# Kernel tuning notes

Measured on AMD Instinct MI355X. Metric: run time of the kernel, lower is better.

The kernel has to match this reference:

```python
import jax, jax.numpy as jnp
import numpy as np

B, D_IN = 16384, 1024
NUM_LAYERS, K, CB_DIM = 4, 1024, 512


def setup_inputs() -> dict:
    key = jax.random.key(0)
    ks = jax.random.split(key, 6)
    return {
        "dense_content_embedding": jax.random.normal(ks[0], (B, D_IN), jnp.float32),
        "enc_W": jax.random.normal(ks[1], (D_IN, CB_DIM), jnp.float32) / np.sqrt(D_IN),
        "enc_b": jnp.zeros((CB_DIM,), jnp.float32),
        "codebooks": jax.random.normal(ks[2], (NUM_LAYERS, K, CB_DIM), jnp.float32),
        "dec_W": jax.random.normal(ks[3], (NUM_LAYERS, CB_DIM), jnp.float32) / np.sqrt(NUM_LAYERS),
        "dec_b": jnp.zeros((CB_DIM,), jnp.float32),
    }


def reference(dense_content_embedding, enc_W, enc_b, codebooks, dec_W, dec_b):
    # encoder: Dense(codebook_dim)
    r0 = dense_content_embedding @ enc_W + enc_b  # [B, CB_DIM]

    def step(residual, cb):
        # squared L2 distance: ||r||^2 - 2 r.c + ||c||^2  -> [B, K]
        d = (jnp.sum(residual * residual, axis=-1, keepdims=True)
             - 2.0 * (residual @ cb.T)
             + jnp.sum(cb * cb, axis=-1))
        idx = jnp.argmin(d, axis=-1)            # [B]
        next_residual = residual - cb[idx]      # gather + residual update
        return next_residual, idx

    _, ids = jax.lax.scan(step, r0, codebooks)  # ids: [L, B]
    semantic_ids = ids.T                        # [B, L] (stack along axis=1)

    # decoder: Dense(codebook_dim) applied to the integer ids (as in source)
    recon = semantic_ids.astype(r0.dtype) @ dec_W + dec_b  # [B, CB_DIM]
    return recon, semantic_ids
```

## Files before the change

### kernel.cpp

```cpp
#include <hip/hip_runtime.h>
#include <float.h>
#include <limits.h>

#define BB 16384
#define DIN 1024
#define CB 512
#define KC 1024
#define NL 4

#define DELTA 0.25f

typedef __attribute__((ext_vector_type(8))) _Float16 half8;
typedef __attribute__((ext_vector_type(8))) short bf16x8;
typedef __attribute__((ext_vector_type(4))) float f32x4;

__device__ __forceinline__ unsigned short f2h(float f) {
  _Float16 h = (_Float16)f;
  return *(unsigned short*)&h;
}

__device__ __forceinline__ unsigned short f2b(float f) {
  unsigned u = __float_as_uint(f);
  unsigned r = u + 0x7fffu + ((u >> 16) & 1u);
  return (unsigned short)(r >> 16);
}
__device__ __forceinline__ float b2f(unsigned short h) {
  return __uint_as_float(((unsigned)h) << 16);
}

__device__ __forceinline__ unsigned cvtpk_bf16(float a, float b) {
  unsigned r;
  asm("v_cvt_pk_bf16_f32 %0, %1, %2" : "=v"(r) : "v"(a), "v"(b));
  return r;
}

__device__ __forceinline__ size_t staged_off(int row, int k) {
  return ((size_t)(row >> 4) * 16 + (k >> 5)) * 512 +
         (((k >> 3) & 3) * 16 + (row & 15)) * 8 + (k & 7);
}

__device__ __forceinline__ size_t staged_off_w(int row, int k) {
  return ((size_t)(row >> 4) * 32 + (k >> 5)) * 512 +
         (((k >> 3) & 3) * 16 + (row & 15)) * 8 + (k & 7);
}


__global__ __launch_bounds__(256) void cbsplit_kernel(
    const float* __restrict__ cbs, unsigned short* __restrict__ Ch16) {
  int g = (blockIdx.x * 256 + threadIdx.x) * 4;
  int k = g & (CB - 1);
  int lr = g >> 9;
  int layer = lr >> 10, row = lr & (KC - 1);
  float4 v = *(const float4*)(cbs + g);
  size_t off = (size_t)layer * (KC / 16) * 8192 + staged_off(row, k);
  *(ushort4*)(Ch16 + off) = make_ushort4(f2h(v.x), f2h(v.y), f2h(v.z), f2h(v.w));
}

__global__ __launch_bounds__(256) void wsplit_kernel(
    const float* __restrict__ W, unsigned short* __restrict__ WTh,
    unsigned short* __restrict__ WTm) {
  int g = blockIdx.x * 256 + threadIdx.x;
  int n = g >> 8;
  int k0 = (g & 255) * 4;
  ushort4 h4, m4;
  unsigned short* hp = (unsigned short*)&h4;
  unsigned short* mp = (unsigned short*)&m4;
#pragma unroll
  for (int i = 0; i < 4; ++i) {
    float x = W[(size_t)(k0 + i) * CB + n];
    unsigned short h = f2b(x);
    hp[i] = h;
    mp[i] = f2b(x - b2f(h));
  }
  size_t off = staged_off_w(n, k0);
  *(ushort4*)(WTh + off) = h4;
  *(ushort4*)(WTm + off) = m4;
}

__global__ __launch_bounds__(256) void cnorm_kernel(
    const float* __restrict__ cbs, double* __restrict__ cnorm,
    float* __restrict__ cnormF) {
  int gw = (blockIdx.x * blockDim.x + threadIdx.x) >> 6;
  int lane = threadIdx.x & 63;
  if (gw >= NL * KC) return;
  const float* row = cbs + (size_t)gw * CB;
  double s = 0.0;
  for (int i = lane; i < CB; i += 64) {
    double v = (double)row[i];
    s += v * v;
  }
#pragma unroll
  for (int off = 32; off > 0; off >>= 1)
    s += __shfl_down(s, off, 64);
  if (lane == 0) { cnorm[gw] = s; cnormF[gw] = (float)s; }
}

__global__ __launch_bounds__(256, 2) void enc_gemm(
    const float* __restrict__ X, const unsigned short* __restrict__ WTh,
    const unsigned short* __restrict__ WTm, const float* __restrict__ bias,
    float* __restrict__ R, unsigned short* __restrict__ Rh16) {
  __shared__ __align__(16) char lds[32768];
  int tid = threadIdx.x;
  int wave = tid >> 6, lane = tid & 63;
  int wm = wave >> 1, wn = wave & 1;
  int q = lane >> 4, l15 = lane & 15;
  int bx = blockIdx.x;
  int rb = ((bx & 7) << 1) + ((bx >> 3) & 1) + ((bx >> 6) << 4);
  int cbk = (bx >> 4) & 3;
  int row0 = rb * 128, n0 = cbk * 128;

  int ar = tid >> 1;
  int aq = (tid & 1) * 16;
  const float* xsrc = X + (size_t)(row0 + ar) * DIN + aq;
  int awoff = (ar >> 4) * 1024 + (((aq >> 3) & 3) * 16 + (ar & 15)) * 16;

  const char* bph = (const char*)WTh +
                    ((size_t)((n0 >> 4) + wn * 4) * 32) * 1024 + lane * 16;
  const char* bpm = (const char*)WTm +
                    ((size_t)((n0 >> 4) + wn * 4) * 32) * 1024 + lane * 16;

  f32x4 acc[4][4];
#pragma unroll
  for (int i = 0; i < 4; ++i)
#pragma unroll
    for (int j = 0; j < 4; ++j)
      acc[i][j] = (f32x4){0.f, 0.f, 0.f, 0.f};

  float xv[16];
  unsigned hp[8], mp[8];
  uint4 BHa[4], BMa[4], BHb[4], BMb[4];

#define LOADX(c)                                         \
  {                                                      \
    _Pragma("unroll") for (int j = 0; j < 4; ++j) {      \
      float4 v = *(const float4*)(xsrc + (c) * 32 + j * 4); \
      xv[4 * j + 0] = v.x; xv[4 * j + 1] = v.y;          \
      xv[4 * j + 2] = v.z; xv[4 * j + 3] = v.w;          \
    }                                                    \
  }
#define SPLITX()                                            \
  {                                                         \
    _Pragma("unroll") for (int j = 0; j < 8; ++j) {         \
      float x0 = xv[2 * j], x1 = xv[2 * j + 1];             \
      unsigned h = cvtpk_bf16(x0, x1);                      \
      float h0 = __uint_as_float(h << 16);                  \
      float h1 = __uint_as_float(h & 0xffff0000u);          \
      hp[j] = h;                                            \
      mp[j] = cvtpk_bf16(x0 - h0, x1 - h1);                 \
    }                                                       \
  }
#define WRITEA(bufbase)                                                     \
  {                                                                         \
    *(uint4*)(lds + (bufbase) + awoff) =                                    \
        make_uint4(hp[0], hp[1], hp[2], hp[3]);                             \
    *(uint4*)(lds + (bufbase) + awoff + 256) =                              \
        make_uint4(hp[4], hp[5], hp[6], hp[7]);                             \
    *(uint4*)(lds + (bufbase) + awoff + 8192) =                             \
        make_uint4(mp[0], mp[1], mp[2], mp[3]);                             \
    *(uint4*)(lds + (bufbase) + awoff + 8192 + 256) =                       \
        make_uint4(mp[4], mp[5], mp[6], mp[7]);                             \
  }
#define BLOADTO(ktile, BH, BM)                                              \
  {                                                                         \
    _Pragma("unroll") for (int tj = 0; tj < 4; ++tj) {                      \
      BH[tj] = *(const uint4*)(bph + (size_t)tj * 32768 + (size_t)(ktile) * 1024); \
      BM[tj] = *(const uint4*)(bpm + (size_t)tj * 32768 + (size_t)(ktile) * 1024); \
    }                                                                       \
  }
#define ESTEP(kt, CB_, NB_, BHc, BMc, BHn, BMn)                             \
  {                                                                         \
    if ((kt) < 31) {                                                        \
      WRITEA(NB_);                                                          \
      BLOADTO((kt) + 1, BHn, BMn);                                          \
    }                                                                       \
    if ((kt) < 30) LOADX((kt) + 2);                                         \
    const char* cb0 = lds + (CB_);                                          \
    bf16x8 ah[4], am[4];                                                    \
    _Pragma("unroll") for (int ti = 0; ti < 4; ++ti) {                      \
      ah[ti] = *(const bf16x8*)(cb0 + (wm * 4 + ti) * 1024 + lane * 16);    \
      am[ti] = *(const bf16x8*)(cb0 + 8192 + (wm * 4 + ti) * 1024 + lane * 16); \
    }                                                                       \
    _Pragma("unroll") for (int tj = 0; tj < 4; ++tj) {                      \
      bf16x8 bh = *(const bf16x8*)&BHc[tj];                                 \
      bf16x8 bm = *(const bf16x8*)&BMc[tj];                                 \
      _Pragma("unroll") for (int ti = 0; ti < 4; ++ti)                      \
        acc[ti][tj] = __builtin_amdgcn_mfma_f32_16x16x32_bf16(ah[ti], bh, acc[ti][tj], 0, 0, 0); \
      _Pragma("unroll") for (int ti = 0; ti < 4; ++ti)                      \
        acc[ti][tj] = __builtin_amdgcn_mfma_f32_16x16x32_bf16(am[ti], bh, acc[ti][tj], 0, 0, 0); \
      _Pragma("unroll") for (int ti = 0; ti < 4; ++ti)                      \
        acc[ti][tj] = __builtin_amdgcn_mfma_f32_16x16x32_bf16(ah[ti], bm, acc[ti][tj], 0, 0, 0); \
    }                                                                       \
    if ((kt) < 30) SPLITX();                                                \
    __syncthreads();                                                        \
  }

  LOADX(0); SPLITX();
  WRITEA(0);
  BLOADTO(0, BHa, BMa);
  LOADX(1); SPLITX();
  __syncthreads();

  for (int kt2 = 0; kt2 < 16; ++kt2) {
    ESTEP(2 * kt2,     0,     16384, BHa, BMa, BHb, BMb);
    ESTEP(2 * kt2 + 1, 16384, 0,     BHb, BMb, BHa, BMa);
  }

#pragma unroll
  for (int ti = 0; ti < 4; ++ti) {
#pragma unroll
    for (int tj = 0; tj < 4; ++tj) {
      int col = n0 + wn * 64 + tj * 16 + l15;
      float bv = bias[col];
#pragma unroll
      for (int r = 0; r < 4; ++r) {
        int row = row0 + wm * 64 + ti * 16 + q * 4 + r;
        float val = acc[ti][tj][r] + bv;
        R[(size_t)row * CB + col] = val;
        Rh16[staged_off(row, col)] = f2h(val);
      }
    }
  }
#undef LOADX
#undef SPLITX
#undef WRITEA
#undef BLOADTO
#undef ESTEP
}

__global__ __launch_bounds__(256, 2) void vq_stage1(
    const unsigned short* __restrict__ Rh16,
    const unsigned short* __restrict__ Ch16,
    const float* __restrict__ cnormF, float4* __restrict__ cand) {
  __shared__ __align__(16) char lds[49152];
  int tid = threadIdx.x;
  int wave = tid >> 6, lane = tid & 63;
  int q = lane >> 4, l15 = lane & 15;
  int g = blockIdx.x;
  int rb = (g & 7) + ((g >> 6) << 3);
  int cbk = (g >> 3) & 7;
  int row0 = rb * 256, n0 = cbk * 128;

  f32x4 acc[4][8];
#pragma unroll
  for (int i = 0; i < 4; ++i)
#pragma unroll
    for (int j = 0; j < 8; ++j)
      acc[i][j] = (f32x4){0.f, 0.f, 0.f, 0.f};

  const unsigned short* gA =
      Rh16 + ((size_t)(row0 >> 4) + wave * 4) * 8192 + lane * 8;
  const unsigned short* gB =
      Ch16 + ((size_t)(n0 >> 4) + wave * 2) * 8192 + lane * 8;
  char* lA = lds + wave * 4 * 1024;
  char* lB = lds + 16384 + wave * 2 * 1024;

#define STAGE1_ISSUE(ktile, bufbase)                                         \
  {                                                                          \
    _Pragma("unroll") for (int s = 0; s < 4; ++s) {                          \
      __builtin_amdgcn_global_load_lds(                                      \
          (const __attribute__((address_space(1))) void*)(                   \
              gA + (size_t)s * 8192 + (ktile) * 512),                        \
          (__attribute__((address_space(3))) void*)(lA + (bufbase) + s * 1024), \
          16, 0, 0);                                                         \
    }                                                                        \
    _Pragma("unroll") for (int s = 0; s < 2; ++s) {                          \
      __builtin_amdgcn_global_load_lds(                                      \
          (const __attribute__((address_space(1))) void*)(                   \
              gB + (size_t)s * 8192 + (ktile) * 512),                        \
          (__attribute__((address_space(3))) void*)(lB + (bufbase) + s * 1024), \
          16, 0, 0);                                                         \
    }                                                                        \
  }

  STAGE1_ISSUE(0, 0);
  __syncthreads();

  for (int kt = 0; kt < 16; ++kt) {
    int cur = kt & 1;
    if (kt < 15) STAGE1_ISSUE(kt + 1, (cur ^ 1) * 24576);
    const char* ca = lds + cur * 24576;
    const char* cbp = ca + 16384;
    half8 af[4];
#pragma unroll
    for (int ri = 0; ri < 4; ++ri)
      af[ri] = *(const half8*)(ca + (wave * 4 + ri) * 1024 + lane * 16);
#pragma unroll
    for (int tj = 0; tj < 8; ++tj) {
      half8 b = *(const half8*)(cbp + tj * 1024 + lane * 16);
#pragma unroll
      for (int ri = 0; ri < 4; ++ri)
        acc[ri][tj] = __builtin_amdgcn_mfma_f32_16x16x32_f16(af[ri], b, acc[ri][tj], 0, 0, 0);
    }
    __syncthreads();
  }
#undef STAGE1_ISSUE

  float cn[8]; int coln[8];
#pragma unroll
  for (int tj = 0; tj < 8; ++tj) {
    coln[tj] = n0 + tj * 16 + l15;
    cn[tj] = cnormF[coln[tj]];
  }
#pragma unroll
  for (int ri = 0; ri < 4; ++ri) {
#pragma unroll
    for (int r = 0; r < 4; ++r) {
      unsigned long long k1 = ~0ull, k2 = ~0ull;
#pragma unroll
      for (int tj = 0; tj < 8; ++tj) {
        float v = cn[tj] - 2.0f * acc[ri][tj][r];
        unsigned u = __float_as_uint(v);
        u = (u & 0x80000000u) ? ~u : (u | 0x80000000u);
        unsigned long long key =
            ((unsigned long long)u << 32) | (unsigned)coln[tj];
        if (key < k1) { k2 = k1; k1 = key; }
        else if (key < k2) { k2 = key; }
      }
#pragma unroll
      for (int mask = 1; mask <= 8; mask <<= 1) {
        unsigned long long o1 = __shfl_xor(k1, mask, 64);
        unsigned long long o2 = __shfl_xor(k2, mask, 64);
        if (o1 < k1) { k2 = (k1 < o2) ? k1 : o2; k1 = o1; }
        else { k2 = (k2 < o1) ? k2 : o1; }
      }
      if (l15 == 0) {
        unsigned s1 = (unsigned)(k1 >> 32), s2 = (unsigned)(k2 >> 32);
        unsigned b1 = (s1 & 0x80000000u) ? (s1 ^ 0x80000000u) : ~s1;
        unsigned b2 = (s2 & 0x80000000u) ? (s2 ^ 0x80000000u) : ~s2;
        int row = row0 + wave * 64 + ri * 16 + q * 4 + r;
        cand[(size_t)row * 8 + cbk] = make_float4(
            __uint_as_float(b1), __int_as_float((int)(unsigned)k1),
            __uint_as_float(b2), __int_as_float((int)(unsigned)k2));
      }
    }
  }
}

__global__ __launch_bounds__(256) void vq_refine(
    const float* __restrict__ cb, const double* __restrict__ cnorm,
    const float4* __restrict__ cand, float* __restrict__ R,
    unsigned short* __restrict__ Rh16, float* __restrict__ idsF, int layer,
    const float* __restrict__ decW, const float* __restrict__ decb,
    float* __restrict__ recon) {
  __shared__ int sIdx[32][16];
  __shared__ int sCnt[32];
  __shared__ int sBest[32];
  __shared__ int sPair[512];
  __shared__ int sNP;
  __shared__ double sD[32][16];

  int tid = threadIdx.x;
  int b = blockIdx.x;
  int v = ((b & 7) << 3) + ((b >> 3) & 7) + ((b >> 6) << 6);
  int row0 = v * 32;

  if (tid == 0) sNP = 0;
  __syncthreads();

  if (tid < 32) {
    int row = row0 + tid;
    float vv[16]; int ix[16];
#pragma unroll
    for (int c = 0; c < 8; ++c) {
      float4 e = cand[(size_t)row * 8 + c];
      vv[2 * c] = e.x;     ix[2 * c] = __float_as_int(e.y);
      vv[2 * c + 1] = e.z; ix[2 * c + 1] = __float_as_int(e.w);
    }
    float M = FLT_MAX; int I = INT_MAX;
#pragma unroll
    for (int p = 0; p < 16; ++p)
      if (vv[p] < M || (vv[p] == M && ix[p] < I)) { M = vv[p]; I = ix[p]; }
    int cnt = 0;
#pragma unroll
    for (int p = 0; p < 16; ++p)
      if (vv[p] < M + DELTA && cnt < 16) sIdx[tid][cnt++] = ix[p];
    sCnt[tid] = cnt;
    sBest[tid] = I;
    if (cnt >= 2) {
      int base = atomicAdd(&sNP, cnt);
      for (int c = 0; c < cnt; ++c) sPair[base + c] = (tid << 4) | c;
    }
  }
  __syncthreads();

  int np = sNP;
  int wave = tid >> 6, lane = tid & 63;
  for (int p = wave; p < np; p += 4) {
    int pr = sPair[p];
    int r = pr >> 4, c = pr & 15;
    int idx = sIdx[r][c];
    const float* rrow = R + (size_t)(row0 + r) * CB;
    const float* crow = cb + (size_t)idx * CB;
    double s = 0.0;
#pragma unroll
    for (int e = 0; e < CB; e += 64)
      s += (double)rrow[e + lane] * (double)crow[e + lane];
#pragma unroll
    for (int off = 32; off > 0; off >>= 1)
      s += __shfl_xor(s, off, 64);
    if (lane == 0) sD[r][c] = cnorm[idx] - 2.0 * s;
  }
  __syncthreads();

  if (tid < 32) {
    int cnt = sCnt[tid];
    if (cnt >= 2) {
      double bestD = 1e300; int bestI = INT_MAX;
      for (int c = 0; c < cnt; ++c) {
        double d = sD[tid][c]; int idx = sIdx[tid][c];
        if (d < bestD || (d == bestD && idx < bestI)) { bestD = d; bestI = idx; }
      }
      sBest[tid] = bestI;
    }
    idsF[(size_t)(row0 + tid) * NL + layer] = (float)sBest[tid];
  }
  __syncthreads();

  if (layer != NL - 1) {
    for (int it = tid; it < 32 * (CB / 4); it += 256) {
      int r = it >> 7, dq = (it & 127) * 4;
      int row = row0 + r;
      size_t o = (size_t)row * CB + dq;
      float4 rv = *(const float4*)(R + o);
      const float* crow = cb + (size_t)sBest[r] * CB + dq;
      float nv[4] = {rv.x - crow[0], rv.y - crow[1], rv.z - crow[2], rv.w - crow[3]};
      *(float4*)(R + o) = make_float4(nv[0], nv[1], nv[2], nv[3]);
      size_t so = staged_off(row, dq);
      *(ushort4*)(Rh16 + so) =
          make_ushort4(f2h(nv[0]), f2h(nv[1]), f2h(nv[2]), f2h(nv[3]));
    }
  } else {
    for (int it = tid; it < 32 * (CB / 4); it += 256) {
      int r = it >> 7, j0 = (it & 127) * 4;
      int row = row0 + r;
      float id3 = (float)sBest[r];
      float out[4];
#pragma unroll
      for (int e = 0; e < 4; ++e) {
        int j = j0 + e;
        float s = decb[j];
#pragma unroll
        for (int l = 0; l < NL - 1; ++l)
          s += idsF[(size_t)row * NL + l] * decW[l * CB + j];
        s += id3 * decW[(NL - 1) * CB + j];
        out[e] = s;
      }
      *(float4*)(recon + (size_t)row * CB + j0) =
          make_float4(out[0], out[1], out[2], out[3]);
    }
  }
}

extern "C" void kernel_launch(void* const* d_in, const int* in_sizes, int n_in,
                              void* d_out, int out_size, void* d_ws, size_t ws_size,
                              hipStream_t stream) {
  const float* X    = (const float*)d_in[0];
  const float* encW = (const float*)d_in[1];
  const float* encb = (const float*)d_in[2];
  const float* cbs  = (const float*)d_in[3];
  const float* decW = (const float*)d_in[4];
  const float* decb = (const float*)d_in[5];

  float* out = (float*)d_out;
  float* recon = out;
  float* idsF = out + (size_t)BB * CB;

  char* ws = (char*)d_ws;
  float* R = (float*)ws;                     ws += (size_t)BB * CB * 4;
  unsigned short* Rh16 = (unsigned short*)ws; ws += (size_t)BB * CB * 2;
  unsigned short* Ch16 = (unsigned short*)ws; ws += (size_t)NL * KC * CB * 2;
  double* cnorm = (double*)ws;               ws += (size_t)NL * KC * 8;
  float* cnormF = (float*)ws;                ws += (size_t)NL * KC * 4;
  float4* cand = (float4*)ws;                ws += (size_t)BB * 8 * 16;
  unsigned short* WTh = (unsigned short*)ws; ws += (size_t)CB * DIN * 2;
  unsigned short* WTm = (unsigned short*)ws;

  cbsplit_kernel<<<(NL * KC * CB) / 1024, 256, 0, stream>>>(cbs, Ch16);
  cnorm_kernel<<<(NL * KC) / 4, 256, 0, stream>>>(cbs, cnorm, cnormF);
  wsplit_kernel<<<(CB * DIN / 4) / 256, 256, 0, stream>>>(encW, WTh, WTm);
  enc_gemm<<<(BB / 128) * (CB / 128), 256, 0, stream>>>(X, WTh, WTm, encb, R, Rh16);
  for (int l = 0; l < NL; ++l) {
    const float* cbl = cbs + (size_t)l * KC * CB;
    vq_stage1<<<(BB / 256) * 8, 256, 0, stream>>>(
        Rh16, Ch16 + (size_t)l * KC * CB, cnormF + (size_t)l * KC, cand);
    vq_refine<<<BB / 32, 256, 0, stream>>>(cbl, cnorm + (size_t)l * KC, cand,
                                           R, Rh16, idsF, l, decW, decb, recon);
  }
}
```

Before: 358.6 us.

## Load stage-1 MFMA operands directly from global into registers, dropping LDS staging

The vq_stage1 distance GEMM no longer stages A and B tiles through double-buffered shared memory with global_load_lds and block barriers. Each wave now loads its own fragments straight from global memory into registers, using register double buffering across k-tiles. This removes the LDS traffic and per-iteration __syncthreads. The cost is that every wave loads the full 128-column B tile itself, which raises global/L2 traffic roughly fourfold for B, and it adds register pressure (24 extra uint4 per thread) under launch_bounds(256,2).

```diff
diff --git a/kernel.cpp b/kernel.cpp
--- a/kernel.cpp
+++ b/kernel.cpp
@@ -231,7 +231,6 @@
     const unsigned short* __restrict__ Rh16,
     const unsigned short* __restrict__ Ch16,
     const float* __restrict__ cnormF, float4* __restrict__ cand) {
-  __shared__ __align__(16) char lds[49152];
   int tid = threadIdx.x;
   int wave = tid >> 6, lane = tid & 63;
   int q = lane >> 4, l15 = lane & 15;
@@ -247,53 +246,48 @@
     for (int j = 0; j < 8; ++j)
       acc[i][j] = (f32x4){0.f, 0.f, 0.f, 0.f};
 
-  const unsigned short* gA =
-      Rh16 + ((size_t)(row0 >> 4) + wave * 4) * 8192 + lane * 8;
-  const unsigned short* gB =
-      Ch16 + ((size_t)(n0 >> 4) + wave * 2) * 8192 + lane * 8;
-  char* lA = lds + wave * 4 * 1024;
-  char* lB = lds + 16384 + wave * 2 * 1024;
-
-#define STAGE1_ISSUE(ktile, bufbase)                                         \
+  const char* aptr = (const char*)Rh16 +
+                     ((size_t)(row0 >> 4) + wave * 4) * 16384 + lane * 16;
+  const char* bptr = (const char*)Ch16 +
+                     ((size_t)(n0 >> 4)) * 16384 + lane * 16;
+
+  uint4 Aa[4], Ab[4];
+  uint4 Ba[8], Bb[8];
+
+#define ALOADTO(ktile, A)                                                    \
   {                                                                          \
-    _Pragma("unroll") for (int s = 0; s < 4; ++s) {                          \
-      __builtin_amdgcn_global_load_lds(                                      \
-          (const __attribute__((address_space(1))) void*)(                   \
-              gA + (size_t)s * 8192 + (ktile) * 512),                        \
-          (__attribute__((address_space(3))) void*)(lA + (bufbase) + s * 1024), \
-          16, 0, 0);                                                         \
+    _Pragma("unroll") for (int ri = 0; ri < 4; ++ri)                         \
+      A[ri] = *(const uint4*)(aptr + (size_t)ri * 16384 + (size_t)(ktile) * 1024); \
+  }
+#define BLOADTO(ktile, B)                                                    \
+  {                                                                          \
+    _Pragma("unroll") for (int tj = 0; tj < 8; ++tj)                         \
+      B[tj] = *(const uint4*)(bptr + (size_t)tj * 16384 + (size_t)(ktile) * 1024); \
+  }
+#define S1STEP(kt, Ac, Bc, An, Bn)                                           \
+  {                                                                          \
+    if ((kt) < 15) {                                                         \
+      ALOADTO((kt) + 1, An);                                                 \
+      BLOADTO((kt) + 1, Bn);                                                 \
     }                                                                        \
-    _Pragma("unroll") for (int s = 0; s < 2; ++s) {                          \
-      __builtin_amdgcn_global_load_lds(                                      \
-          (const __attribute__((address_space(1))) void*)(                   \
-              gB + (size_t)s * 8192 + (ktile) * 512),                        \
-          (__attribute__((address_space(3))) void*)(lB + (bufbase) + s * 1024), \
-          16, 0, 0);                                                         \
+    _Pragma("unroll") for (int tj = 0; tj < 8; ++tj) {                       \
+      half8 b = *(const half8*)&Bc[tj];                                      \
+      _Pragma("unroll") for (int ri = 0; ri < 4; ++ri)                       \
+        acc[ri][tj] = __builtin_amdgcn_mfma_f32_16x16x32_f16(                \
+            *(const half8*)&Ac[ri], b, acc[ri][tj], 0, 0, 0);                \
     }                                                                        \
   }
 
-  STAGE1_ISSUE(0, 0);
-  __syncthreads();
-
-  for (int kt = 0; kt < 16; ++kt) {
-    int cur = kt & 1;
-    if (kt < 15) STAGE1_ISSUE(kt + 1, (cur ^ 1) * 24576);
-    const char* ca = lds + cur * 24576;
-    const char* cbp = ca + 16384;
-    half8 af[4];
-#pragma unroll
-    for (int ri = 0; ri < 4; ++ri)
-      af[ri] = *(const half8*)(ca + (wave * 4 + ri) * 1024 + lane * 16);
-#pragma unroll
-    for (int tj = 0; tj < 8; ++tj) {
-      half8 b = *(const half8*)(cbp + tj * 1024 + lane * 16);
-#pragma unroll
-      for (int ri = 0; ri < 4; ++ri)
-        acc[ri][tj] = __builtin_amdgcn_mfma_f32_16x16x32_f16(af[ri], b, acc[ri][tj], 0, 0, 0);
-    }
-    __syncthreads();
-  }
-#undef STAGE1_ISSUE
+  ALOADTO(0, Aa);
+  BLOADTO(0, Ba);
+
+  for (int kt2 = 0; kt2 < 8; ++kt2) {
+    S1STEP(2 * kt2,     Aa, Ba, Ab, Bb);
+    S1STEP(2 * kt2 + 1, Ab, Bb, Aa, Ba);
+  }
+#undef ALOADTO
+#undef BLOADTO
+#undef S1STEP
 
   float cn[8]; int coln[8];
 #pragma unroll
```

New measurement: 362.3 us. About the same (+1.0%).
